# Performance work log

Measured on AMD Instinct MI355X. Metric: run time of the kernel, lower is better.

Reference implementation:

```python
import jax, jax.numpy as jnp
import numpy as np

K = 16  # neighbors per node (dgl.knn_graph k)


def _knn_indices(centers, k):
    # pairwise squared distances [N, N]
    sq = jnp.sum(centers * centers, axis=1)
    d2 = sq[:, None] + sq[None, :] - 2.0 * (centers @ centers.T)
    # k nearest (includes self at distance ~0), edges: neighbor(src) -> node(dst)
    _, idx = jax.lax.top_k(-d2, k)  # [N, k]
    return idx


def _graph_conv(h, idx, src_norm, dst_norm, W, b):
    # DGL GraphConv, norm='both': D_out^{-1/2} A D_in^{-1/2} H W + b
    hs = h * src_norm[:, None]          # scale by out-degree^{-1/2}
    agg = jnp.sum(hs[idx], axis=1)      # sum over k neighbors -> [N, F]
    agg = agg * dst_norm                # in-degree is exactly k for knn graph
    return agg @ W + b


def setup_inputs() -> dict:
    key = jax.random.key(0)
    ks = jax.random.split(key, 8)
    N, D, H = 20000, 128, 256
    s_in, s_h = 1.0 / np.sqrt(D), 1.0 / np.sqrt(H)
    return {
        "x": jax.random.normal(ks[0], (N, D), dtype=jnp.float32),
        "centers": jax.random.normal(ks[1], (N, 3), dtype=jnp.float32),
        "W0": jax.random.normal(ks[2], (D, H), dtype=jnp.float32) * s_in,
        "b0": jnp.zeros((H,), dtype=jnp.float32),
        "W1": jax.random.normal(ks[3], (H, H), dtype=jnp.float32) * s_h,
        "b1": jnp.zeros((H,), dtype=jnp.float32),
        "W2": jax.random.normal(ks[4], (H, H), dtype=jnp.float32) * s_h,
        "b2": jnp.zeros((H,), dtype=jnp.float32),
        "Wf": jax.random.normal(ks[5], (H, 1), dtype=jnp.float32) * s_h,
        "bf": jnp.zeros((1,), dtype=jnp.float32),
    }


def reference(x, centers, W0, b0, W1, b1, W2, b2, Wf, bf):
    N = x.shape[0]
    idx = _knn_indices(centers, K)  # [N, K] src nodes per dst node
    # out-degree of each node = number of times it appears as a neighbor
    out_deg = jnp.zeros((N,), dtype=x.dtype).at[idx.reshape(-1)].add(1.0)
    src_norm = jax.lax.rsqrt(jnp.maximum(out_deg, 1.0))
    dst_norm = 1.0 / jnp.sqrt(jnp.asarray(K, dtype=x.dtype))  # in-degree == K
    h = x
    for W, b in ((W0, b0), (W1, b1), (W2, b2)):
        h = jax.nn.relu(_graph_conv(h, idx, src_norm, dst_norm, W, b))
    logits = (h @ Wf + bf).squeeze(-1)  # [N]
    return jax.nn.sigmoid(logits)
```

## Files before the change

kernel.cpp:

```cpp
#include <hip/hip_runtime.h>
#include <math.h>

#define KNN 16
#define G 16
#define G3 4096
#define MRING 15
#define FLTMAX 3.402823466e+38f

typedef __attribute__((ext_vector_type(8))) short short8x;
typedef __attribute__((ext_vector_type(4))) float f32x4;

__device__ __forceinline__ unsigned short bf16rn(float x) {
  unsigned u = __float_as_uint(x);
  unsigned r = (u + 0x7FFFu + ((u >> 16) & 1u)) >> 16;
  return (unsigned short)r;
}
__device__ __forceinline__ float bf16tof(unsigned short h) {
  return __uint_as_float(((unsigned)h) << 16);
}

__device__ __forceinline__ unsigned fkey(float f) {
  unsigned u = __float_as_uint(f);
  return (u & 0x80000000u) ? ~u : (u | 0x80000000u);
}
__device__ __forceinline__ float funkey(unsigned u) {
  unsigned b = (u & 0x80000000u) ? (u & 0x7FFFFFFFu) : ~u;
  return __uint_as_float(b);
}

__device__ __forceinline__ void cell_of(float x, float y, float z, const float* P,
                                        int& cx, int& cy, int& cz) {
  cx = min(G - 1, max(0, (int)((x - P[0]) * P[3])));
  cy = min(G - 1, max(0, (int)((y - P[1]) * P[4])));
  cz = min(G - 1, max(0, (int)((z - P[2]) * P[5])));
}

__global__ void prep_kernel(const float* __restrict__ centers,
                            float4* __restrict__ cpack, int* __restrict__ deg,
                            int* __restrict__ counts, int* __restrict__ cursor,
                            int n) {
  #pragma clang fp contract(off)
  int t = blockIdx.x * blockDim.x + threadIdx.x;
  if (t < G3) counts[t] = 0;
  else if (t < 2 * G3) cursor[t - G3] = 0;
  if (t < n) {
    float x = centers[3 * t], y = centers[3 * t + 1], z = centers[3 * t + 2];
    float sq = (x * x + y * y) + z * z;
    cpack[t] = make_float4(x, y, z, sq);
    deg[t] = 0;
  }
}

__global__ __launch_bounds__(1024) void params_kernel(const float4* __restrict__ cpack,
                                                      float* __restrict__ P, int n) {
  __shared__ float sminb[16][3], smaxb[16][3];
  int tid = threadIdx.x;
  float mnx = FLTMAX, mny = FLTMAX, mnz = FLTMAX;
  float mxx = -FLTMAX, mxy = -FLTMAX, mxz = -FLTMAX;
  for (int i = tid; i < n; i += 1024) {
    float4 c = cpack[i];
    mnx = fminf(mnx, c.x); mny = fminf(mny, c.y); mnz = fminf(mnz, c.z);
    mxx = fmaxf(mxx, c.x); mxy = fmaxf(mxy, c.y); mxz = fmaxf(mxz, c.z);
  }
  #pragma unroll
  for (int off = 1; off < 64; off <<= 1) {
    mnx = fminf(mnx, __shfl_xor(mnx, off));
    mny = fminf(mny, __shfl_xor(mny, off));
    mnz = fminf(mnz, __shfl_xor(mnz, off));
    mxx = fmaxf(mxx, __shfl_xor(mxx, off));
    mxy = fmaxf(mxy, __shfl_xor(mxy, off));
    mxz = fmaxf(mxz, __shfl_xor(mxz, off));
  }
  if ((tid & 63) == 0) {
    int w = tid >> 6;
    sminb[w][0] = mnx; sminb[w][1] = mny; sminb[w][2] = mnz;
    smaxb[w][0] = mxx; smaxb[w][1] = mxy; smaxb[w][2] = mxz;
  }
  __syncthreads();
  if (tid == 0) {
    float xmin = sminb[0][0], ymin = sminb[0][1], zmin = sminb[0][2];
    float xmax = smaxb[0][0], ymax = smaxb[0][1], zmax = smaxb[0][2];
    for (int w = 1; w < 16; ++w) {
      xmin = fminf(xmin, sminb[w][0]); ymin = fminf(ymin, sminb[w][1]);
      zmin = fminf(zmin, sminb[w][2]);
      xmax = fmaxf(xmax, smaxb[w][0]); ymax = fmaxf(ymax, smaxb[w][1]);
      zmax = fmaxf(zmax, smaxb[w][2]);
    }
    float ex = fmaxf(xmax - xmin, 1e-9f);
    float ey = fmaxf(ymax - ymin, 1e-9f);
    float ez = fmaxf(zmax - zmin, 1e-9f);
    P[0] = xmin; P[1] = ymin; P[2] = zmin;
    P[3] = (float)G / ex; P[4] = (float)G / ey; P[5] = (float)G / ez;
    P[6] = ex / (float)G; P[7] = ey / (float)G; P[8] = ez / (float)G;
    P[9] = fminf(P[6], fminf(P[7], P[8]));
  }
}

__global__ void count_kernel(const float4* __restrict__ cpack, const float* __restrict__ P,
                             int* __restrict__ counts, int n) {
  int i = blockIdx.x * blockDim.x + threadIdx.x;
  if (i >= n) return;
  float4 c = cpack[i];
  int cx, cy, cz; cell_of(c.x, c.y, c.z, P, cx, cy, cz);
  atomicAdd(&counts[(cz * G + cy) * G + cx], 1);
}

__global__ __launch_bounds__(1024) void scan_kernel(const int* __restrict__ counts,
                                                    int* __restrict__ starts,
                                                    int2* __restrict__ cellinfo) {
  __shared__ int sh[1024];
  int t = threadIdx.x;
  int base = t * 4;
  int loc[4];
  int cnts[4];
  int s = 0;
  #pragma unroll
  for (int u = 0; u < 4; ++u) {
    cnts[u] = counts[base + u];
    loc[u] = s; s += cnts[u];
  }
  sh[t] = s;
  __syncthreads();
  for (int off = 1; off < 1024; off <<= 1) {
    int v = (t >= off) ? sh[t - off] : 0;
    __syncthreads();
    sh[t] += v;
    __syncthreads();
  }
  int pre = (t == 0) ? 0 : sh[t - 1];
  #pragma unroll
  for (int u = 0; u < 4; ++u) {
    int st = pre + loc[u];
    starts[base + u] = st;
    cellinfo[base + u] = make_int2(st, cnts[u]);
  }
}

__global__ void scatter_kernel(const float4* __restrict__ cpack, const float* __restrict__ P,
                               const int* __restrict__ starts, int* __restrict__ cursor,
                               int* __restrict__ sid, int* __restrict__ inv,
                               float4* __restrict__ spack, int n) {
  int i = blockIdx.x * blockDim.x + threadIdx.x;
  if (i >= n) return;
  float4 c = cpack[i];
  int cx, cy, cz; cell_of(c.x, c.y, c.z, P, cx, cy, cz);
  int cell = (cz * G + cy) * G + cx;
  int slot = starts[cell] + atomicAdd(&cursor[cell], 1);
  sid[slot] = i;
  inv[i] = slot;
  spack[slot] = c;
}

__global__ __launch_bounds__(64) void query_kernel(
    const float4* __restrict__ spack, const int* __restrict__ sid,
    const int* __restrict__ inv, const int2* __restrict__ cellinfo,
    const float* __restrict__ P, int* __restrict__ knn_idx,
    int* __restrict__ deg, int n) {
  #pragma clang fp contract(off)
  __shared__ unsigned long long lsk[KNN][64];
  const int lane = threadIdx.x;
  const int g = blockIdx.x;
  if (g >= n) return;
  const float4 q = spack[g];
  const float xmin = P[0], ymin = P[1], zmin = P[2];
  const float wx = P[6], wy = P[7], wz = P[8], wmin = P[9];
  int cx, cy, cz; cell_of(q.x, q.y, q.z, P, cx, cy, cz);

  int cnt = 0;
  unsigned long long wkey = 0; int wslot = 0;
  unsigned long long minkey = ~0ull; int minslot = 0;

  for (int m = 1; m <= MRING; ++m) {
    if (m >= 2) {
      float b = (float)(m - 1) * wmin;
      float b2 = b * b * 0.999f;
      unsigned long long tk = ((unsigned long long)fkey(b2)) << 32;
      int c = 0;
      for (int t = 0; t < cnt; ++t) c += (lsk[t][lane] < tk) ? 1 : 0;
      #pragma unroll
      for (int off = 1; off < 64; off <<= 1) c += __shfl_xor(c, off);
      if (c >= KNN) break;
    }
    float lw = (cnt == KNN) ? funkey((unsigned)(wkey >> 32)) : FLTMAX;
    #pragma unroll
    for (int off = 1; off < 64; off <<= 1) lw = fminf(lw, __shfl_xor(lw, off));
    const bool do_prune = (lw < FLTMAX);

    const int ncells = (m == 1) ? 27 : (24 * m * m + 2);
    for (int cb = 0; cb < ncells; cb += 64) {
      int f = cb + lane;
      int ccnt = 0, cs0 = 0;
      if (f < ncells) {
        int dx, dy, dz;
        if (m == 1) {
          dz = f / 9 - 1; int rem = f % 9; dy = rem / 3 - 1; dx = rem % 3 - 1;
        } else {
          int side = 2 * m + 1;
          int S1 = side * side;
          if (f < 2 * S1) {
            dz = (f < S1) ? -m : m;
            int i2 = (f < S1) ? f : f - S1;
            dy = i2 / side - m; dx = i2 % side - m;
          } else {
            int r = f - 2 * S1;
            int layer = r / (8 * m);
            int t2 = r - layer * 8 * m;
            dz = layer - (m - 1);
            if (t2 < side) { dy = -m; dx = t2 - m; }
            else if (t2 < 2 * side) { dy = m; dx = (t2 - side) - m; }
            else { int u = t2 - 2 * side; dx = (u & 1) ? m : -m; dy = (u >> 1) - (m - 1); }
          }
        }
        int x = cx + dx, y = cy + dy, z = cz + dz;
        if (x >= 0 && x < G && y >= 0 && y < G && z >= 0 && z < G) {
          int cell = (z * G + y) * G + x;
          int2 ci = cellinfo[cell];
          if (ci.y > 0) {
            bool pass = true;
            if (do_prune) {
              float lox = xmin + (float)x * wx;
              float loy = ymin + (float)y * wy;
              float loz = zmin + (float)z * wz;
              float ddx = fmaxf(fmaxf(lox - q.x, q.x - (lox + wx)), 0.f);
              float ddy = fmaxf(fmaxf(loy - q.y, q.y - (loy + wy)), 0.f);
              float ddz = fmaxf(fmaxf(loz - q.z, q.z - (loz + wz)), 0.f);
              float cd2 = ddx * ddx + ddy * ddy + ddz * ddz;
              pass = !(cd2 * 0.999f > lw);
            }
            if (pass) { ccnt = ci.y; cs0 = ci.x; }
          }
        }
      }
      int inc = ccnt;
      #pragma unroll
      for (int off = 1; off < 64; off <<= 1) {
        int t = __shfl_up(inc, off);
        if (lane >= off) inc += t;
      }
      int total = __shfl(inc, 63);
      if (total == 0) continue;
      unsigned seg = ((unsigned)(inc - ccnt) << 16) | (unsigned)cs0;
      const int tmax = total - 1;

      int fc = lane;
      int fcc = min(fc, tmax);
      int lo = 0;
      #pragma unroll
      for (int s = 32; s >= 1; s >>= 1) {
        int cand = lo + s;
        unsigned o = __shfl(seg, cand & 63);
        if (cand < 64 && (int)(o >> 16) <= fcc) lo = cand;
      }
      unsigned o2 = __shfl(seg, lo);
      int src = (int)(o2 & 0xFFFFu) + (fcc - (int)(o2 >> 16));
      float4 c4 = spack[src];
      int j = sid[src];
      const int nloop = (total + 63) >> 6;
      for (int it = 0; it < nloop; ++it) {
        int fn = fc + 64;
        int fnc = min(fn, tmax);
        int lo2 = 0;
        #pragma unroll
        for (int s = 32; s >= 1; s >>= 1) {
          int cand = lo2 + s;
          unsigned o = __shfl(seg, cand & 63);
          if (cand < 64 && (int)(o >> 16) <= fnc) lo2 = cand;
        }
        unsigned o3 = __shfl(seg, lo2);
        int srcn = (int)(o3 & 0xFFFFu) + (fnc - (int)(o3 >> 16));
        float4 c4n = spack[srcn];
        int jn = sid[srcn];
        if (fc < total) {
          float dot = fmaf(q.z, c4.z, fmaf(q.y, c4.y, q.x * c4.x));
          float d2 = (q.w + c4.w) - 2.0f * dot;
          unsigned long long key =
              (((unsigned long long)fkey(d2)) << 32) | (unsigned)j;
          if (cnt < KNN) {
            lsk[cnt][lane] = key;
            if (key < minkey) { minkey = key; minslot = cnt; }
            ++cnt;
            if (cnt == KNN) {
              wkey = 0; wslot = 0;
              #pragma unroll
              for (int u = 0; u < KNN; ++u) {
                unsigned long long k2 = lsk[u][lane];
                if (k2 > wkey) { wkey = k2; wslot = u; }
              }
            }
          } else if (key < wkey) {
            lsk[wslot][lane] = key;
            if (key < minkey) { minkey = key; minslot = wslot; }
            wkey = 0;
            #pragma unroll
            for (int u = 0; u < KNN; ++u) {
              unsigned long long k2 = lsk[u][lane];
              if (k2 > wkey) { wkey = k2; wslot = u; }
            }
          }
        }
        fc = fn; c4 = c4n; j = jn;
      }
    }
  }

  unsigned long long mykey = 0;
  for (int t = 0; t < KNN; ++t) {
    unsigned long long k = minkey; int src = lane;
    #pragma unroll
    for (int off = 1; off < 64; off <<= 1) {
      unsigned long long ok = __shfl_xor(k, off);
      int os = __shfl_xor(src, off);
      if (ok < k) { k = ok; src = os; }
    }
    if (lane == t) mykey = k;
    if (lane == src) {
      lsk[minslot][lane] = ~0ull;
      minkey = ~0ull; minslot = 0;
      for (int u = 0; u < cnt; ++u) {
        unsigned long long kk = lsk[u][lane];
        if (kk < minkey) { minkey = kk; minslot = u; }
      }
    }
  }
  if (lane < KNN) {
    int j = (int)(unsigned)(mykey & 0xFFFFFFFFull);
    int js = inv[j];
    knn_idx[g * KNN + lane] = js;
    atomicAdd(&deg[js], 1);
  }
}

__global__ void norm_kernel(const int* __restrict__ deg, float* __restrict__ srcn, int n) {
  int i = blockIdx.x * blockDim.x + threadIdx.x;
  if (i < n) {
    float d = (float)max(deg[i], 1);
    srcn[i] = 1.0f / sqrtf(d);
  }
}

__global__ void split_w_kernel(const float* __restrict__ W,
                               unsigned short* __restrict__ wbh,
                               unsigned short* __restrict__ wbl, int K) {
  int t = blockIdx.x * blockDim.x + threadIdx.x;
  int noct = (K >> 5) * 1024;
  if (t >= noct) return;
  int kblk = t >> 10;
  int g = (t >> 6) & 15;
  int l = t & 63;
  int n = ((g >> 2) << 6) + ((g & 3) << 4) + (l & 15);
  int kbase = (kblk << 5) + ((l >> 4) << 3);
  #pragma unroll
  for (int j = 0; j < 8; ++j) {
    float w = W[(kbase + j) * 256 + n];
    unsigned short hi = bf16rn(w);
    wbh[t * 8 + j] = hi;
    wbl[t * 8 + j] = bf16rn(w - bf16tof(hi));
  }
}

__device__ __forceinline__ int xcd_swizzle(int b, int grid8) {
  int nch = grid8 >> 3;
  return (b & 7) * nch + (b >> 3);
}

template <int F>
__global__ __launch_bounds__(256) void agg_kernel(const float* __restrict__ h,
                                                  const int* __restrict__ rmap,
                                                  const float* __restrict__ srcn,
                                                  const int* __restrict__ idx,
                                                  unsigned short* __restrict__ ah,
                                                  unsigned short* __restrict__ al,
                                                  int n) {
  const int lane = threadIdx.x & 63;
  const int wv = threadIdx.x >> 6;
  const int eb = xcd_swizzle(blockIdx.x, gridDim.x);
  const int i = eb * 4 + wv;
  if (i >= n) return;
  constexpr int V = F / 64;
  if constexpr (V == 4) {
    float4 acc = make_float4(0.f, 0.f, 0.f, 0.f);
    #pragma unroll
    for (int k = 0; k < KNN; ++k) {
      int s = idx[i * KNN + k];
      float sn = srcn[s];
      int row = rmap ? rmap[s] : s;
      float4 hv = ((const float4*)(h + (size_t)row * F))[lane];
      acc.x = fmaf(sn, hv.x, acc.x);
      acc.y = fmaf(sn, hv.y, acc.y);
      acc.z = fmaf(sn, hv.z, acc.z);
      acc.w = fmaf(sn, hv.w, acc.w);
    }
    acc.x *= 0.25f; acc.y *= 0.25f; acc.z *= 0.25f; acc.w *= 0.25f;
    ushort4 hh, ll;
    hh.x = bf16rn(acc.x); ll.x = bf16rn(acc.x - bf16tof(hh.x));
    hh.y = bf16rn(acc.y); ll.y = bf16rn(acc.y - bf16tof(hh.y));
    hh.z = bf16rn(acc.z); ll.z = bf16rn(acc.z - bf16tof(hh.z));
    hh.w = bf16rn(acc.w); ll.w = bf16rn(acc.w - bf16tof(hh.w));
    ((ushort4*)(ah + (size_t)i * F))[lane] = hh;
    ((ushort4*)(al + (size_t)i * F))[lane] = ll;
  } else {
    float2 acc = make_float2(0.f, 0.f);
    #pragma unroll
    for (int k = 0; k < KNN; ++k) {
      int s = idx[i * KNN + k];
      float sn = srcn[s];
      int row = rmap ? rmap[s] : s;
      float2 hv = ((const float2*)(h + (size_t)row * F))[lane];
      acc.x = fmaf(sn, hv.x, acc.x);
      acc.y = fmaf(sn, hv.y, acc.y);
    }
    acc.x *= 0.25f; acc.y *= 0.25f;
    ushort2 hh, ll;
    hh.x = bf16rn(acc.x); ll.x = bf16rn(acc.x - bf16tof(hh.x));
    hh.y = bf16rn(acc.y); ll.y = bf16rn(acc.y - bf16tof(hh.y));
    ((ushort2*)(ah + (size_t)i * F))[lane] = hh;
    ((ushort2*)(al + (size_t)i * F))[lane] = ll;
  }
}

__global__ __launch_bounds__(256) void gemm_mfma(
    const unsigned short* __restrict__ ah, const unsigned short* __restrict__ al,
    const unsigned short* __restrict__ wbh, const unsigned short* __restrict__ wbl,
    const float* __restrict__ bias, float* __restrict__ C, int M, int Kd,
    const float* __restrict__ Wf, const float* __restrict__ bfp,
    const int* __restrict__ sid, float* __restrict__ outp) {
  __shared__ unsigned short sa_h[2][64][8];
  __shared__ unsigned short sa_l[2][64][8];
  __shared__ unsigned short sb_h[16][64][8];
  __shared__ unsigned short sb_l[16][64][8];
  __shared__ float fred[32][4];
  const int tid = threadIdx.x;
  const int lane = tid & 63;
  const int w = tid >> 6;
  const int eb = xcd_swizzle(blockIdx.x, gridDim.x);
  const int mt0 = eb * 32;
  if (mt0 >= M) return;

  f32x4 acc[2][4];
  #pragma unroll
  for (int ms = 0; ms < 2; ++ms)
    #pragma unroll
    for (int ns = 0; ns < 4; ++ns) acc[ms][ns] = (f32x4){0.f, 0.f, 0.f, 0.f};

  const int nkb = Kd >> 5;
  for (int kit = 0; kit < nkb; ++kit) {
    const int k0 = kit << 5;
    if (tid < 128) {
      int msub = tid >> 6, l = tid & 63;
      int row = mt0 + (msub << 4) + (l & 15);
      int kk = k0 + ((l >> 4) << 3);
      if (row < M) {
        *(uint4*)&sa_h[msub][l][0] = *(const uint4*)(ah + (size_t)row * Kd + kk);
        *(uint4*)&sa_l[msub][l][0] = *(const uint4*)(al + (size_t)row * Kd + kk);
      } else {
        uint4 z = make_uint4(0, 0, 0, 0);
        *(uint4*)&sa_h[msub][l][0] = z;
        *(uint4*)&sa_l[msub][l][0] = z;
      }
    }
    #pragma unroll
    for (int o = tid; o < 1024; o += 256) {
      size_t off = ((size_t)kit * 1024 + o) * 8;
      *(uint4*)&sb_h[o >> 6][o & 63][0] = *(const uint4*)(wbh + off);
      *(uint4*)&sb_l[o >> 6][o & 63][0] = *(const uint4*)(wbl + off);
    }
    __syncthreads();
    short8x a_h0 = *(const short8x*)&sa_h[0][lane][0];
    short8x a_h1 = *(const short8x*)&sa_h[1][lane][0];
    short8x a_l0 = *(const short8x*)&sa_l[0][lane][0];
    short8x a_l1 = *(const short8x*)&sa_l[1][lane][0];
    #pragma unroll
    for (int ns = 0; ns < 4; ++ns) {
      short8x b_h = *(const short8x*)&sb_h[w * 4 + ns][lane][0];
      short8x b_l = *(const short8x*)&sb_l[w * 4 + ns][lane][0];
      acc[0][ns] = __builtin_amdgcn_mfma_f32_16x16x32_bf16(a_h0, b_h, acc[0][ns], 0, 0, 0);
      acc[0][ns] = __builtin_amdgcn_mfma_f32_16x16x32_bf16(a_h0, b_l, acc[0][ns], 0, 0, 0);
      acc[0][ns] = __builtin_amdgcn_mfma_f32_16x16x32_bf16(a_l0, b_h, acc[0][ns], 0, 0, 0);
      acc[1][ns] = __builtin_amdgcn_mfma_f32_16x16x32_bf16(a_h1, b_h, acc[1][ns], 0, 0, 0);
      acc[1][ns] = __builtin_amdgcn_mfma_f32_16x16x32_bf16(a_h1, b_l, acc[1][ns], 0, 0, 0);
      acc[1][ns] = __builtin_amdgcn_mfma_f32_16x16x32_bf16(a_l1, b_h, acc[1][ns], 0, 0, 0);
    }
    __syncthreads();
  }

  const int col = lane & 15;
  const int rq = lane >> 4;
  if (Wf) {
    float pr[2][4];
    #pragma unroll
    for (int ms = 0; ms < 2; ++ms)
      #pragma unroll
      for (int r = 0; r < 4; ++r) pr[ms][r] = 0.f;
    #pragma unroll
    for (int ns = 0; ns < 4; ++ns) {
      int nn = (w << 6) + (ns << 4) + col;
      float bi = bias[nn];
      float wv = Wf[nn];
      #pragma unroll
      for (int ms = 0; ms < 2; ++ms)
        #pragma unroll
        for (int r = 0; r < 4; ++r)
          pr[ms][r] = fmaf(fmaxf(acc[ms][ns][r] + bi, 0.f), wv, pr[ms][r]);
    }
    #pragma unroll
    for (int mask = 1; mask < 16; mask <<= 1)
      #pragma unroll
      for (int ms = 0; ms < 2; ++ms)
        #pragma unroll
        for (int r = 0; r < 4; ++r) pr[ms][r] += __shfl_xor(pr[ms][r], mask);
    if (col == 0) {
      #pragma unroll
      for (int ms = 0; ms < 2; ++ms)
        #pragma unroll
        for (int r = 0; r < 4; ++r) fred[(ms << 4) + (rq << 2) + r][w] = pr[ms][r];
    }
    __syncthreads();
    if (tid < 32) {
      int row = mt0 + tid;
      if (row < M) {
        float s = ((fred[tid][0] + fred[tid][1]) + (fred[tid][2] + fred[tid][3])) + bfp[0];
        outp[sid[row]] = 1.0f / (1.0f + expf(-s));
      }
    }
  } else {
    #pragma unroll
    for (int ms = 0; ms < 2; ++ms) {
      #pragma unroll
      for (int ns = 0; ns < 4; ++ns) {
        int nn = (w << 6) + (ns << 4) + col;
        float bi = bias[nn];
        #pragma unroll
        for (int r = 0; r < 4; ++r) {
          int row = mt0 + (ms << 4) + (rq << 2) + r;
          if (row < M) C[(size_t)row * 256 + nn] = fmaxf(acc[ms][ns][r] + bi, 0.f);
        }
      }
    }
  }
}

extern "C" void kernel_launch(void* const* d_in, const int* in_sizes, int n_in,
                              void* d_out, int out_size, void* d_ws, size_t ws_size,
                              hipStream_t stream) {
  const float* x = (const float*)d_in[0];
  const float* centers = (const float*)d_in[1];
  const float* W0 = (const float*)d_in[2];
  const float* b0 = (const float*)d_in[3];
  const float* W1 = (const float*)d_in[4];
  const float* b1 = (const float*)d_in[5];
  const float* W2 = (const float*)d_in[6];
  const float* b2 = (const float*)d_in[7];
  const float* Wf = (const float*)d_in[8];
  const float* bf = (const float*)d_in[9];
  float* out = (float*)d_out;

  const int N = in_sizes[1] / 3;

  char* p = (char*)d_ws;
  auto alloc = [&](size_t bytes) {
    void* r = (void*)p;
    p += (bytes + 255) & ~(size_t)255;
    return r;
  };
  float4* cpack = (float4*)alloc((size_t)N * 16);
  int* deg = (int*)alloc((size_t)N * 4);
  float* srcn = (float*)alloc((size_t)N * 4);
  int* idx = (int*)alloc((size_t)N * KNN * 4);
  unsigned short* ahb = (unsigned short*)alloc((size_t)N * 256 * 2);
  unsigned short* alb = (unsigned short*)alloc((size_t)N * 256 * 2);
  float* hA = (float*)alloc((size_t)N * 256 * 4);
  float* P = (float*)alloc(16 * 4);
  int* counts = (int*)alloc((size_t)G3 * 4);
  int* starts = (int*)alloc((size_t)G3 * 4);
  int* cursor = (int*)alloc((size_t)G3 * 4);
  int2* cellinfo = (int2*)alloc((size_t)G3 * 8);
  int* sid = (int*)alloc((size_t)N * 4);
  int* inv = (int*)alloc((size_t)N * 4);
  float4* spack = (float4*)alloc((size_t)N * 16);
  unsigned short* w0h = (unsigned short*)alloc(128 * 256 * 2);
  unsigned short* w0l = (unsigned short*)alloc(128 * 256 * 2);
  unsigned short* w1h = (unsigned short*)alloc(256 * 256 * 2);
  unsigned short* w1l = (unsigned short*)alloc(256 * 256 * 2);
  unsigned short* w2h = (unsigned short*)alloc(256 * 256 * 2);
  unsigned short* w2l = (unsigned short*)alloc(256 * 256 * 2);
  (void)ws_size; (void)n_in; (void)out_size;

  const int nb = (N + 255) / 256;

  prep_kernel<<<256, 256, 0, stream>>>(centers, cpack, deg, counts, cursor, N);
  split_w_kernel<<<(128 / 32) * 1024 / 256, 256, 0, stream>>>(W0, w0h, w0l, 128);
  split_w_kernel<<<(256 / 32) * 1024 / 256, 256, 0, stream>>>(W1, w1h, w1l, 256);
  split_w_kernel<<<(256 / 32) * 1024 / 256, 256, 0, stream>>>(W2, w2h, w2l, 256);
  params_kernel<<<1, 1024, 0, stream>>>(cpack, P, N);
  count_kernel<<<nb, 256, 0, stream>>>(cpack, P, counts, N);
  scan_kernel<<<1, 1024, 0, stream>>>(counts, starts, cellinfo);
  scatter_kernel<<<nb, 256, 0, stream>>>(cpack, P, starts, cursor, sid, inv, spack, N);
  query_kernel<<<N, 64, 0, stream>>>(spack, sid, inv, cellinfo, P, idx, deg, N);
  norm_kernel<<<nb, 256, 0, stream>>>(deg, srcn, N);

  const int agrid = ((N + 3) / 4 + 7) & ~7;
  const int ggrid = (((N + 31) / 32) + 7) & ~7;

  agg_kernel<128><<<agrid, 256, 0, stream>>>(x, sid, srcn, idx, ahb, alb, N);
  gemm_mfma<<<ggrid, 256, 0, stream>>>(ahb, alb, w0h, w0l, b0, hA, N, 128,
                                       nullptr, nullptr, nullptr, nullptr);

  agg_kernel<256><<<agrid, 256, 0, stream>>>(hA, nullptr, srcn, idx, ahb, alb, N);
  gemm_mfma<<<ggrid, 256, 0, stream>>>(ahb, alb, w1h, w1l, b1, hA, N, 256,
                                       nullptr, nullptr, nullptr, nullptr);

  agg_kernel<256><<<agrid, 256, 0, stream>>>(hA, nullptr, srcn, idx, ahb, alb, N);
  gemm_mfma<<<ggrid, 256, 0, stream>>>(ahb, alb, w2h, w2l, b2, nullptr, N, 256,
                                       Wf, bf, sid, out);
}
```

Baseline: 438.6 us.

## Replace serial 16-round wavefront min-extraction with threshold filter and rank sort

The final top-16 selection in the kNN query kernel previously ran 16 rounds of wave-wide 64-bit shuffle min reductions, each followed by a per-lane rescan. It now keeps only candidates below the ring-termination threshold, compacts them into shared memory with a prefix scan, and finds each survivor's position with a parallel rank count. This removes the serial shuffle chain at the cost of an O(Tp^2) rank loop and extra barriers. If the loop finishes without the early break, the threshold stays at its maximum and all candidates are ranked. Correctness also relies on exactly the first 16 ranks being unique, which holds because the keys carry the point index.

```diff
diff --git a/kernel.cpp b/kernel.cpp
--- a/kernel.cpp
+++ b/kernel.cpp
@@ -158,6 +158,7 @@
     int* __restrict__ deg, int n) {
   #pragma clang fp contract(off)
   __shared__ unsigned long long lsk[KNN][64];
+  __shared__ unsigned long long outk[KNN];
   const int lane = threadIdx.x;
   const int g = blockIdx.x;
   if (g >= n) return;
@@ -168,7 +169,7 @@
 
   int cnt = 0;
   unsigned long long wkey = 0; int wslot = 0;
-  unsigned long long minkey = ~0ull; int minslot = 0;
+  unsigned long long tkf = ~0ull;
 
   for (int m = 1; m <= MRING; ++m) {
     if (m >= 2) {
@@ -179,7 +180,7 @@
       for (int t = 0; t < cnt; ++t) c += (lsk[t][lane] < tk) ? 1 : 0;
       #pragma unroll
       for (int off = 1; off < 64; off <<= 1) c += __shfl_xor(c, off);
-      if (c >= KNN) break;
+      if (c >= KNN) { tkf = tk; break; }
     }
     float lw = (cnt == KNN) ? funkey((unsigned)(wkey >> 32)) : FLTMAX;
     #pragma unroll
@@ -277,7 +278,6 @@
               (((unsigned long long)fkey(d2)) << 32) | (unsigned)j;
           if (cnt < KNN) {
             lsk[cnt][lane] = key;
-            if (key < minkey) { minkey = key; minslot = cnt; }
             ++cnt;
             if (cnt == KNN) {
               wkey = 0; wslot = 0;
@@ -289,7 +289,6 @@
             }
           } else if (key < wkey) {
             lsk[wslot][lane] = key;
-            if (key < minkey) { minkey = key; minslot = wslot; }
             wkey = 0;
             #pragma unroll
             for (int u = 0; u < KNN; ++u) {
@@ -303,27 +302,37 @@
     }
   }
 
-  unsigned long long mykey = 0;
-  for (int t = 0; t < KNN; ++t) {
-    unsigned long long k = minkey; int src = lane;
-    #pragma unroll
-    for (int off = 1; off < 64; off <<= 1) {
-      unsigned long long ok = __shfl_xor(k, off);
-      int os = __shfl_xor(src, off);
-      if (ok < k) { k = ok; src = os; }
-    }
-    if (lane == t) mykey = k;
-    if (lane == src) {
-      lsk[minslot][lane] = ~0ull;
-      minkey = ~0ull; minslot = 0;
-      for (int u = 0; u < cnt; ++u) {
-        unsigned long long kk = lsk[u][lane];
-        if (kk < minkey) { minkey = kk; minslot = u; }
-      }
-    }
-  }
+  unsigned long long* flat = &lsk[0][0];
+  unsigned long long mykeys[KNN];
+  #pragma unroll
+  for (int u = 0; u < KNN; ++u) mykeys[u] = lsk[u][lane];
+  int fcnt = 0;
+  #pragma unroll
+  for (int u = 0; u < KNN; ++u) fcnt += (u < cnt && mykeys[u] < tkf) ? 1 : 0;
+  int pre = fcnt;
+  #pragma unroll
+  for (int off = 1; off < 64; off <<= 1) {
+    int t = __shfl_up(pre, off);
+    if (lane >= off) pre += t;
+  }
+  const int Tp = __shfl(pre, 63);
+  const int base = pre - fcnt;
+  __syncthreads();
+  int wptr = 0;
+  #pragma unroll
+  for (int u = 0; u < KNN; ++u) {
+    if (u < cnt && mykeys[u] < tkf) { flat[base + wptr] = mykeys[u]; ++wptr; }
+  }
+  __syncthreads();
+  for (int s = lane; s < Tp; s += 64) {
+    unsigned long long ks = flat[s];
+    int rank = 0;
+    for (int t = 0; t < Tp; ++t) rank += (flat[t] < ks) ? 1 : 0;
+    if (rank < KNN) outk[rank] = ks;
+  }
+  __syncthreads();
   if (lane < KNN) {
-    int j = (int)(unsigned)(mykey & 0xFFFFFFFFull);
+    int j = (int)(unsigned)(outk[lane] & 0xFFFFFFFFull);
     int js = inv[j];
     knn_idx[g * KNN + lane] = js;
     atomicAdd(&deg[js], 1);
```

Result: slower. 461.9 us (+5.3%).
